# Kernel tuning notes

Hardware: AMD Instinct MI355X
Metric: run time of the kernel (lower is better)

Reference implementation:

```python
import jax, jax.numpy as jnp
import numpy as np

B, N, IN_DIM, HID, K = 32, 512, 1024, 512, 3
ALPHA = 0.2  # leaky_relu negative slope
NEG = -9e15


def setup_inputs() -> dict:
    key = jax.random.key(0)
    ks = jax.random.split(key, 7)
    hidden_states = jax.random.normal(ks[0], (B, N, IN_DIM), jnp.float32)
    adj = (jax.random.uniform(ks[1], (B, 3, N, N)) < 0.05).astype(jnp.float32)
    W_all = jax.random.normal(ks[2], (3, K, IN_DIM, HID), jnp.float32) * 0.02
    a_all = jax.random.normal(ks[3], (3, K, 2 * HID, 1), jnp.float32) * 0.02
    wawa_w = jax.random.normal(ks[4], (HID, 100), jnp.float32) * 0.05
    wawa_b = jnp.zeros((100,), jnp.float32)
    ctx_w = jax.random.normal(ks[5], (100, 1), jnp.float32) * 0.05
    return {"hidden_states": hidden_states, "adj": adj, "W_all": W_all,
            "a_all": a_all, "wawa_w": wawa_w, "wawa_b": wawa_b, "ctx_w": ctx_w}


def _gat(adj_m, x, W, a):
    # e_ij = leaky_relu(cat[h_i, h_j] @ a) == leaky_relu(h_i@a1 + h_j@a2)
    h = jnp.einsum('bnf,fh->bnh', x, W)           # [B,N,HID]
    f1 = jnp.einsum('bnh,ho->bno', h, a[:HID])    # [B,N,1]
    f2 = jnp.einsum('bnh,ho->bno', h, a[HID:])    # [B,N,1]
    e = jax.nn.leaky_relu(f1 + jnp.swapaxes(f2, 1, 2), negative_slope=ALPHA)  # [B,N,N]
    att = jnp.where(adj_m > 0, e, NEG)
    att = jax.nn.softmax(att, axis=2)
    return jnp.einsum('bnm,bmh->bnh', att, h)


def reference(hidden_states, adj, W_all, a_all, wawa_w, wawa_b, ctx_w):
    adj_a, adj_b, adj_c = adj[:, 0], adj[:, 1], adj[:, 2]
    pa, pb, pc = adj_a, adj_b, adj_c  # matmuls(A, k) = A^(k+1)
    hs = []
    for layer in range(K):
        if layer > 0:
            pa = jnp.matmul(pa, adj_a)
            pb = jnp.matmul(pb, adj_b)
            pc = jnp.matmul(pc, adj_c)
        h_layer = (_gat(pa, hidden_states, W_all[0, layer], a_all[0, layer])
                   + _gat(pb, hidden_states, W_all[1, layer], a_all[1, layer])
                   + _gat(pc, hidden_states, W_all[2, layer], a_all[2, layer]))
        hs.append(h_layer)
    # attention-based combination over the K orders
    s = [jnp.einsum('bnc,co->bno', jnp.tanh(jnp.einsum('bnh,hc->bnc', h, wawa_w) + wawa_b), ctx_w)
         for h in hs]                              # each [B,N,1]
    vs = jax.nn.softmax(jnp.concatenate(s, axis=2), axis=2)  # [B,N,K]
    h_stack = jnp.stack(hs, axis=2)                # [B,N,K,HID]
    return jnp.sum(vs[..., None] * h_stack, axis=2)  # [B,N,HID]
```

## Files before the change

kernel.cpp:

```cpp
#include <hip/hip_runtime.h>
#include <hip/hip_bf16.h>

typedef short v8s __attribute__((ext_vector_type(8)));
typedef float v4f __attribute__((ext_vector_type(4)));
typedef unsigned long long u64;

#define ALPHA 0.2f

__device__ inline unsigned short f32_bf16(float x){
    unsigned int u = __float_as_uint(x);
    unsigned int r = (u + 0x7fffu + ((u >> 16) & 1u)) >> 16;
    return (unsigned short)r;
}
__device__ inline float bf16_f32(unsigned short s){
    return __uint_as_float(((unsigned int)s) << 16);
}
__device__ inline v4f mfma16(v8s a, v8s b, v4f c){
    return __builtin_amdgcn_mfma_f32_16x16x32_bf16(a, b, c, 0, 0, 0);
}
__device__ inline void gload16(const unsigned short* g, short* l){
    __builtin_amdgcn_global_load_lds((const __attribute__((address_space(1))) unsigned int*)g,
                                     (__attribute__((address_space(3))) unsigned int*)l,
                                     16, 0, 0);
}


__global__ void k_convert_x(const float* __restrict__ x, v8s* __restrict__ out, int n8){
    int i = blockIdx.x * 256 + threadIdx.x;
    if (i >= n8) return;
    const float4* p = (const float4*)x + (size_t)i * 2;
    float4 a = p[0], b = p[1];
    v8s r;
    r[0] = (short)f32_bf16(a.x); r[1] = (short)f32_bf16(a.y);
    r[2] = (short)f32_bf16(a.z); r[3] = (short)f32_bf16(a.w);
    r[4] = (short)f32_bf16(b.x); r[5] = (short)f32_bf16(b.y);
    r[6] = (short)f32_bf16(b.z); r[7] = (short)f32_bf16(b.w);
    out[i] = r;
}

__global__ void k_transpose_w(const float* __restrict__ W, unsigned short* __restrict__ Wt){
    __shared__ float tile[32][33];
    int g = blockIdx.z, k0 = blockIdx.x * 32, h0 = blockIdx.y * 32;
    int tx = threadIdx.x, ty = threadIdx.y;
    #pragma unroll
    for (int i = 0; i < 4; ++i)
        tile[ty + i*8][tx] = W[((size_t)g*1024 + k0 + ty + i*8)*512 + h0 + tx];
    __syncthreads();
    #pragma unroll
    for (int i = 0; i < 4; ++i){
        int h = ty + i*8;
        Wt[((size_t)g*512 + h0 + h)*1024 + k0 + tx] = f32_bf16(tile[tx][h]);
    }
}

__global__ void k_wawat(const float* __restrict__ w, unsigned short* __restrict__ wt){
    int i = blockIdx.x * 256 + threadIdx.x;
    if (i >= 128 * 512) return;
    int c = i >> 9, k = i & 511;
    wt[i] = (c < 100) ? f32_bf16(w[k*100 + c]) : (unsigned short)0;
}


__global__ __launch_bounds__(256) void k_bits(const float* __restrict__ adj,
                                              u64* __restrict__ bits){
    int row = blockIdx.x * 4 + (threadIdx.x >> 6);
    int t = row >> 14, b = (row >> 9) & 31, i = row & 511;
    const float* src = adj + (((size_t)b*3 + t)*512 + i)*512;
    int lane = threadIdx.x & 63;
    #pragma unroll
    for (int w = 0; w < 8; ++w){
        u64 word = __ballot(src[w*64 + lane] > 0.5f);
        if (lane == 0) bits[(size_t)row*8 + w] = word;
    }
}

__global__ __launch_bounds__(256) void k_boolmm(const u64* __restrict__ prev,
                                                const u64* __restrict__ base,
                                                u64* __restrict__ out){
    int row = blockIdx.x * 256 + threadIdx.x;
    if (row >= 49152) return;
    int tb = row >> 9;
    const u64* pr = prev + (size_t)row * 8;
    const u64* bb = base + ((size_t)tb << 9) * 8;
    ulonglong2 a0 = {0,0}, a1 = {0,0}, a2 = {0,0}, a3 = {0,0};
    #pragma unroll
    for (int w = 0; w < 8; ++w){
        u64 m = pr[w];
        const u64* bw = bb + (size_t)(w << 6) * 8;
        while (m){
            int k = __builtin_ctzll(m);
            m &= m - 1;
            const ulonglong2* br = (const ulonglong2*)(bw + (size_t)k * 8);
            ulonglong2 b0 = br[0], b1 = br[1], b2 = br[2], b3 = br[3];
            a0.x |= b0.x; a0.y |= b0.y;
            a1.x |= b1.x; a1.y |= b1.y;
            a2.x |= b2.x; a2.y |= b2.y;
            a3.x |= b3.x; a3.y |= b3.y;
        }
    }
    ulonglong2* op = (ulonglong2*)(out + (size_t)row * 8);
    op[0] = a0; op[1] = a1; op[2] = a2; op[3] = a3;
}

__global__ __launch_bounds__(256, 4) void k_gemm_h(
    const unsigned short* __restrict__ Wt, const unsigned short* __restrict__ Xb,
    unsigned short* __restrict__ Ht, const float* __restrict__ aall,
    float* __restrict__ f1p, float* __restrict__ f2p, int l)
{
    __shared__ __align__(16) short As[128*32];
    __shared__ __align__(16) short As2[128*32];
    __shared__ __align__(16) short Bs[128*32];
    __shared__ __align__(16) short Bs2[128*32];
    const int bn = blockIdx.x, bm = blockIdx.y, t = blockIdx.z;
    const int g = t*3 + l;
    const int tid = threadIdx.x;
    const int lane = tid & 63, wave = tid >> 6;
    const int wr = wave >> 1, wc = wave & 1;
    const int fr = lane & 15, fq = lane >> 4;
    const int slot = fq ^ (fr & 3) ^ ((fr >> 2) & 3);

    const int srow = tid >> 2, sw = tid & 3;
    const int gw = sw ^ (srow & 3) ^ ((srow >> 2) & 3);
    const unsigned short* Ap = Wt + ((size_t)g*512 + (size_t)bm*128 + srow)*1024 + gw*8;
    const unsigned short* Bp = Xb + ((size_t)bn*128 + srow)*1024 + gw*8;
    short* AsW  = As  + wave*512;
    short* As2W = As2 + wave*512;
    short* BsW  = Bs  + wave*512;
    short* Bs2W = Bs2 + wave*512;

    v4f acc[4][4] = {};

    for (int kt = 0; kt < 16; ++kt){
        const unsigned short* a0 = Ap + kt*64;
        const unsigned short* b0 = Bp + kt*64;
        gload16(a0,                AsW);
        gload16(a0 + 64*1024,      AsW  + 2048);
        gload16(b0,                BsW);
        gload16(b0 + 64*1024,      BsW  + 2048);
        gload16(a0 + 32,           As2W);
        gload16(a0 + 32 + 64*1024, As2W + 2048);
        gload16(b0 + 32,           Bs2W);
        gload16(b0 + 32 + 64*1024, Bs2W + 2048);
        __syncthreads();
        {
            v8s af[4], bf[4];
            #pragma unroll
            for (int i = 0; i < 4; ++i) af[i] = *(const v8s*)&As[(wr*64 + i*16 + fr)*32 + slot*8];
            #pragma unroll
            for (int i = 0; i < 4; ++i) bf[i] = *(const v8s*)&Bs[(wc*64 + i*16 + fr)*32 + slot*8];
            #pragma unroll
            for (int i = 0; i < 4; ++i)
                #pragma unroll
                for (int j = 0; j < 4; ++j)
                    acc[i][j] = mfma16(af[i], bf[j], acc[i][j]);
        }
        {
            v8s af[4], bf[4];
            #pragma unroll
            for (int i = 0; i < 4; ++i) af[i] = *(const v8s*)&As2[(wr*64 + i*16 + fr)*32 + slot*8];
            #pragma unroll
            for (int i = 0; i < 4; ++i) bf[i] = *(const v8s*)&Bs2[(wc*64 + i*16 + fr)*32 + slot*8];
            #pragma unroll
            for (int i = 0; i < 4; ++i)
                #pragma unroll
                for (int j = 0; j < 4; ++j)
                    acc[i][j] = mfma16(af[i], bf[j], acc[i][j]);
        }
        __syncthreads();
    }
    #pragma unroll
    for (int i = 0; i < 4; ++i){
        const int h = bm*128 + wr*64 + i*16 + fq*4;
        #pragma unroll
        for (int j = 0; j < 4; ++j){
            const int mc = bn*128 + wc*64 + j*16 + fr;
            unsigned short* dst = Ht + ((size_t)t*512 + h)*16384 + mc;
            #pragma unroll
            for (int rg = 0; rg < 4; ++rg)
                dst[(size_t)rg*16384] = f32_bf16(acc[i][j][rg]);
        }
    }
    const float* a1 = aall + ((size_t)t*3 + l)*1024;
    const float* a2 = a1 + 512;
    float s1[4] = {0.f,0.f,0.f,0.f}, s2[4] = {0.f,0.f,0.f,0.f};
    #pragma unroll
    for (int i = 0; i < 4; ++i){
        #pragma unroll
        for (int rg = 0; rg < 4; ++rg){
            const int h = bm*128 + wr*64 + i*16 + fq*4 + rg;
            const float c1 = a1[h], c2 = a2[h];
            #pragma unroll
            for (int j = 0; j < 4; ++j){
                s1[j] += acc[i][j][rg]*c1;
                s2[j] += acc[i][j][rg]*c2;
            }
        }
    }
    #pragma unroll
    for (int j = 0; j < 4; ++j){
        s1[j] += __shfl_xor(s1[j], 16); s1[j] += __shfl_xor(s1[j], 32);
        s2[j] += __shfl_xor(s2[j], 16); s2[j] += __shfl_xor(s2[j], 32);
    }
    float* scr = (float*)As;
    __syncthreads();
    if (fq == 0){
        #pragma unroll
        for (int j = 0; j < 4; ++j){
            scr[(((wr*2 + wc)*4 + j)*16 + fr)*2 + 0] = s1[j];
            scr[(((wr*2 + wc)*4 + j)*16 + fr)*2 + 1] = s2[j];
        }
    }
    __syncthreads();
    if (tid < 256){
        const int which = tid & 1, fr2 = (tid >> 1) & 15, j2 = (tid >> 5) & 3,
                  wc2 = (tid >> 7) & 1;
        const float v = scr[(((0*2 + wc2)*4 + j2)*16 + fr2)*2 + which]
                      + scr[(((1*2 + wc2)*4 + j2)*16 + fr2)*2 + which];
        const int m = bn*128 + wc2*64 + j2*16 + fr2;
        float* dst = which ? f2p : f1p;
        dst[((size_t)bm*3 + t)*16384 + m] = v;
    }
}

__global__ __launch_bounds__(256) void k_soft(
    const float* __restrict__ f1p, const float* __restrict__ f2p,
    const u64* __restrict__ maskP, unsigned short* __restrict__ att)
{
    const int row = blockIdx.x * 4 + (threadIdx.x >> 6);
    const int lane = threadIdx.x & 63;
    const int tb = row >> 9;
    const int t = tb >> 5, b = tb & 31;
    const int m1 = b*512 + (row & 511);
    float f1v = 0.f;
    #pragma unroll
    for (int bm = 0; bm < 4; ++bm)
        f1v += f1p[((size_t)bm*3 + t)*16384 + m1];
    const u64 mword = maskP[(size_t)row*8 + (lane >> 3)];
    const unsigned int mbits = (unsigned int)((mword >> ((lane & 7)*8)) & 0xffu);
    const int m2 = b*512 + lane*8;
    float f2v[8] = {0.f,0.f,0.f,0.f,0.f,0.f,0.f,0.f};
    #pragma unroll
    for (int bm = 0; bm < 4; ++bm){
        const float4* fp = (const float4*)(f2p + ((size_t)bm*3 + t)*16384 + m2);
        float4 fa = fp[0], fb = fp[1];
        f2v[0] += fa.x; f2v[1] += fa.y; f2v[2] += fa.z; f2v[3] += fa.w;
        f2v[4] += fb.x; f2v[5] += fb.y; f2v[6] += fb.z; f2v[7] += fb.w;
    }
    float p[8];
    float sm = 0.f;
    #pragma unroll
    for (int u = 0; u < 8; ++u){
        float e = f1v + f2v[u];
        e = (e >= 0.f) ? e : ALPHA*e;
        float pe = (mbits & (1u << u)) ? __expf(e) : 0.f;
        p[u] = pe; sm += pe;
    }
    sm += __shfl_xor(sm, 1);  sm += __shfl_xor(sm, 2);  sm += __shfl_xor(sm, 4);
    sm += __shfl_xor(sm, 8);  sm += __shfl_xor(sm, 16); sm += __shfl_xor(sm, 32);
    const float rinv = 1.f / (sm + 1e-30f);
    v8s pk;
    #pragma unroll
    for (int u = 0; u < 8; ++u) pk[u] = (short)f32_bf16(p[u] * rinv);
    *(v8s*)&att[(size_t)row*512 + lane*8] = pk;
}

__global__ __launch_bounds__(256, 4) void k_pv(
    const unsigned short* __restrict__ att, const unsigned short* __restrict__ Ht,
    unsigned short* __restrict__ hlb)
{
    __shared__ __align__(16) short As[128*32];
    __shared__ __align__(16) short As2[128*32];
    __shared__ __align__(16) short Bs[128*32];
    __shared__ __align__(16) short Bs2[128*32];
    const int b = blockIdx.x, hc = blockIdx.y, rt = blockIdx.z;
    const int tid = threadIdx.x;
    const int lane = tid & 63, wave = tid >> 6;
    const int wr = wave >> 1, wc = wave & 1;
    const int fr = lane & 15, fq = lane >> 4;
    const int slot = fq ^ (fr & 3) ^ ((fr >> 2) & 3);
    const int srow = tid >> 2, sw = tid & 3;
    const int gw = sw ^ (srow & 3) ^ ((srow >> 2) & 3);
    short* AsW  = As  + wave*512;
    short* As2W = As2 + wave*512;
    short* BsW  = Bs  + wave*512;
    short* Bs2W = Bs2 + wave*512;

    v4f acc[4][4] = {};

    for (int t = 0; t < 3; ++t){
        const unsigned short* Ap = att + ((size_t)((t*32 + b)*512 + rt*128 + srow))*512 + gw*8;
        const unsigned short* Bp = Ht + ((size_t)t*512 + hc*128 + srow)*16384 + (size_t)b*512 + gw*8;
        for (int kk = 0; kk < 8; ++kk){
            const unsigned short* a0 = Ap + kk*64;
            const unsigned short* b0 = Bp + kk*64;
            gload16(a0,                         AsW);
            gload16(a0 + 64*512,                AsW  + 2048);
            gload16(b0,                         BsW);
            gload16(b0 + (size_t)64*16384,      BsW  + 2048);
            gload16(a0 + 32,                    As2W);
            gload16(a0 + 32 + 64*512,           As2W + 2048);
            gload16(b0 + 32,                    Bs2W);
            gload16(b0 + 32 + (size_t)64*16384, Bs2W + 2048);
            __syncthreads();
            {
                v8s af[4], bf[4];
                #pragma unroll
                for (int i = 0; i < 4; ++i) af[i] = *(const v8s*)&As[(wr*64 + i*16 + fr)*32 + slot*8];
                #pragma unroll
                for (int j = 0; j < 4; ++j) bf[j] = *(const v8s*)&Bs[(wc*64 + j*16 + fr)*32 + slot*8];
                #pragma unroll
                for (int i = 0; i < 4; ++i)
                    #pragma unroll
                    for (int j = 0; j < 4; ++j)
                        acc[i][j] = mfma16(af[i], bf[j], acc[i][j]);
            }
            {
                v8s af[4], bf[4];
                #pragma unroll
                for (int i = 0; i < 4; ++i) af[i] = *(const v8s*)&As2[(wr*64 + i*16 + fr)*32 + slot*8];
                #pragma unroll
                for (int j = 0; j < 4; ++j) bf[j] = *(const v8s*)&Bs2[(wc*64 + j*16 + fr)*32 + slot*8];
                #pragma unroll
                for (int i = 0; i < 4; ++i)
                    #pragma unroll
                    for (int j = 0; j < 4; ++j)
                        acc[i][j] = mfma16(af[i], bf[j], acc[i][j]);
            }
            __syncthreads();
        }
    }
    #pragma unroll
    for (int i = 0; i < 4; ++i){
        const int r = rt*128 + wr*64 + i*16 + fq*4;
        #pragma unroll
        for (int j = 0; j < 4; ++j){
            const int h = hc*128 + wc*64 + j*16 + fr;
            unsigned short* d1 = hlb + ((size_t)b*512 + r)*512 + h;
            #pragma unroll
            for (int rg = 0; rg < 4; ++rg)
                d1[(size_t)rg*512] = f32_bf16(acc[i][j][rg]);
        }
    }
}

__global__ __launch_bounds__(256) void k_gemm_s(
    const unsigned short* __restrict__ Hb, const unsigned short* __restrict__ Wwt,
    const float* __restrict__ wb, const float* __restrict__ cw,
    float* __restrict__ s)
{
    __shared__ __align__(16) short As[128*32];
    __shared__ __align__(16) short Bs[128*32];
    const int bm = blockIdx.x;
    const int tid = threadIdx.x;
    const int lane = tid & 63, wave = tid >> 6;
    const int wr = wave >> 1, wc = wave & 1;
    const int fr = lane & 15, fq = lane >> 4;
    const int slot = fq ^ (fr & 3) ^ ((fr >> 2) & 3);
    const int srow = tid >> 2, sw = tid & 3;
    const int gw = sw ^ (srow & 3) ^ ((srow >> 2) & 3);
    const unsigned short* Ap = Hb + ((size_t)bm*128 + srow)*512 + gw*8;
    const unsigned short* Bp = Wwt + (size_t)srow*512 + gw*8;

    v4f acc[4][4] = {};
    v8s ra0 = *(const v8s*)(Ap);
    v8s ra1 = *(const v8s*)(Ap + 64*512);
    v8s rb0 = *(const v8s*)(Bp);
    v8s rb1 = *(const v8s*)(Bp + 64*512);

    for (int kt = 0; kt < 16; ++kt){
        __syncthreads();
        *(v8s*)&As[tid*8]        = ra0;
        *(v8s*)&As[tid*8 + 2048] = ra1;
        *(v8s*)&Bs[tid*8]        = rb0;
        *(v8s*)&Bs[tid*8 + 2048] = rb1;
        __syncthreads();
        if (kt + 1 < 16){
            const unsigned short* An = Ap + (kt+1)*32;
            const unsigned short* Bn = Bp + (kt+1)*32;
            ra0 = *(const v8s*)(An); ra1 = *(const v8s*)(An + 64*512);
            rb0 = *(const v8s*)(Bn); rb1 = *(const v8s*)(Bn + 64*512);
        }
        v8s af[4], bf[4];
        #pragma unroll
        for (int i = 0; i < 4; ++i) af[i] = *(const v8s*)&As[(wr*64 + i*16 + fr)*32 + slot*8];
        #pragma unroll
        for (int i = 0; i < 4; ++i) bf[i] = *(const v8s*)&Bs[(wc*64 + i*16 + fr)*32 + slot*8];
        #pragma unroll
        for (int i = 0; i < 4; ++i)
            #pragma unroll
            for (int j = 0; j < 4; ++j)
                acc[i][j] = mfma16(af[i], bf[j], acc[i][j]);
    }
    float part[4][4];
    #pragma unroll
    for (int i = 0; i < 4; ++i)
        #pragma unroll
        for (int rg = 0; rg < 4; ++rg) part[i][rg] = 0.f;
    #pragma unroll
    for (int j = 0; j < 4; ++j){
        const int c = wc*64 + j*16 + fr;
        const bool valid = (c < 100);
        const float wbc = valid ? wb[c] : 0.f;
        const float cwc = valid ? cw[c] : 0.f;
        #pragma unroll
        for (int i = 0; i < 4; ++i)
            #pragma unroll
            for (int rg = 0; rg < 4; ++rg){
                float x = acc[i][j][rg] + wbc;
                float th;
                if (x > 15.f) th = 1.f;
                else if (x < -15.f) th = -1.f;
                else { float ex = __expf(2.f*x); th = (ex - 1.f) / (ex + 1.f); }
                part[i][rg] += th * cwc;
            }
    }
    #pragma unroll
    for (int i = 0; i < 4; ++i)
        #pragma unroll
        for (int rg = 0; rg < 4; ++rg){
            float v = part[i][rg];
            v += __shfl_xor(v, 1);
            v += __shfl_xor(v, 2);
            v += __shfl_xor(v, 4);
            v += __shfl_xor(v, 8);
            part[i][rg] = v;
        }
    float* scr = (float*)As;
    __syncthreads();
    if (fr == 0){
        #pragma unroll
        for (int i = 0; i < 4; ++i)
            #pragma unroll
            for (int rg = 0; rg < 4; ++rg)
                scr[(wr*64 + i*16 + fq*4 + rg)*2 + wc] = part[i][rg];
    }
    __syncthreads();
    if (tid < 128){
        const float v = scr[tid*2] + scr[tid*2 + 1];
        const int grow = bm*128 + tid;
        s[grow] = v;
    }
}

__global__ void k_comb(const unsigned short* __restrict__ hlb, const float* __restrict__ s,
                       float* __restrict__ out)
{
    int idx = blockIdx.x * 256 + threadIdx.x;
    if (idx >= 16384*64) return;
    int m = idx >> 6, c8 = (idx & 63) << 3;
    float s0 = s[m], s1 = s[16384 + m], s2 = s[32768 + m];
    float m0 = fmaxf(s0, fmaxf(s1, s2));
    float e0 = __expf(s0-m0), e1 = __expf(s1-m0), e2 = __expf(s2-m0);
    float inv = 1.f / (e0 + e1 + e2);
    float v0 = e0*inv, v1 = e1*inv, v2 = e2*inv;
    const unsigned short* hp = hlb + (size_t)m*512 + c8;
    v8s a = *(const v8s*)hp;
    v8s bb = *(const v8s*)(hp + (size_t)16384*512);
    v8s cc = *(const v8s*)(hp + (size_t)2*16384*512);
    float o[8];
    #pragma unroll
    for (int u = 0; u < 8; ++u)
        o[u] = v0*bf16_f32((unsigned short)a[u])
             + v1*bf16_f32((unsigned short)bb[u])
             + v2*bf16_f32((unsigned short)cc[u]);
    float4* dst = (float4*)(out + (size_t)m*512 + c8);
    dst[0] = make_float4(o[0], o[1], o[2], o[3]);
    dst[1] = make_float4(o[4], o[5], o[6], o[7]);
}

extern "C" void kernel_launch(void* const* d_in, const int* in_sizes, int n_in,
                              void* d_out, int out_size, void* d_ws, size_t ws_size,
                              hipStream_t stream)
{
    (void)in_sizes; (void)n_in; (void)out_size; (void)ws_size;
    const float* hs   = (const float*)d_in[0];
    const float* adj  = (const float*)d_in[1];
    const float* W    = (const float*)d_in[2];
    const float* aall = (const float*)d_in[3];
    const float* ww   = (const float*)d_in[4];
    const float* wb   = (const float*)d_in[5];
    const float* cw   = (const float*)d_in[6];
    float* out = (float*)d_out;
    char* ws = (char*)d_ws;

    unsigned short* Xb  = (unsigned short*)(ws);
    unsigned short* Wt  = (unsigned short*)(ws + 33554432);
    unsigned short* Wwt = (unsigned short*)(ws + 42991616);
    u64* bits           = (u64*)(ws + 43122688);
    u64* P2             = (u64*)(ws + 46268416);
    u64* P3             = (u64*)(ws + 49414144);
    unsigned short* Ht  = (unsigned short*)(ws + 52559872);
    float* f1p          = (float*)(ws + 103284736);
    float* f2p          = (float*)(ws + 104071168);
    unsigned short* att = (unsigned short*)(ws + 104857600);
    unsigned short* hlb = (unsigned short*)(ws + 203948032);
    float* sbuf         = (float*)(ws + 52559872);

    k_convert_x<<<8192, 256, 0, stream>>>(hs, (v8s*)Xb, 2097152);
    k_transpose_w<<<dim3(32,16,9), dim3(32,8), 0, stream>>>(W, Wt);
    k_wawat<<<256, 256, 0, stream>>>(ww, Wwt);
    k_bits<<<12288, 256, 0, stream>>>(adj, bits);
    k_boolmm<<<192, 256, 0, stream>>>(bits, bits, P2);
    k_boolmm<<<192, 256, 0, stream>>>(bits, P2, P3);

    const u64* masks[3] = {bits, P2, P3};
    for (int l = 0; l < 3; ++l){
        k_gemm_h<<<dim3(128,4,3), 256, 0, stream>>>(Wt, Xb, Ht, aall, f1p, f2p, l);
        k_soft<<<12288, 256, 0, stream>>>(f1p, f2p, masks[l], att);
        k_pv<<<dim3(32,4,4), 256, 0, stream>>>(att, Ht,
            hlb + (size_t)l*16384*512);
    }
    k_gemm_s<<<384, 256, 0, stream>>>(hlb, Wwt, wb, cw, sbuf);
    k_comb<<<4096, 256, 0, stream>>>(hlb, sbuf, out);
}
```

Baseline: 514.6 us.

## Double-buffer LDS tiles in GEMM and PV kernels to overlap loads with MFMA

Replaces the load-all-then-compute k-loop in k_gemm_h and k_pv with a two-stage ping-pong LDS pipeline. The next 32-wide k-slice is prefetched via global_load_lds while MFMAs run on the current slice, with one vmcnt wait and barrier per step. The t/kk loops in k_pv are flattened into a single 48-step pipeline, and s_setprio raises wave priority around the MFMA block. This hides global-load latency, at the cost of twice as many barriers with half the compute between each, plus hand-placed waitcnt and fences that must keep LDS hazards correct.

```diff
diff --git a/kernel.cpp b/kernel.cpp
--- a/kernel.cpp
+++ b/kernel.cpp
@@ -23,6 +23,8 @@
                                      (__attribute__((address_space(3))) unsigned int*)l,
                                      16, 0, 0);
 }
+#define VMCNT0   asm volatile("s_waitcnt vmcnt(0)" ::: "memory")
+#define CFENCE   asm volatile("" ::: "memory")
 
 
 __global__ void k_convert_x(const float* __restrict__ x, v8s* __restrict__ out, int n8){
@@ -107,10 +109,10 @@
     unsigned short* __restrict__ Ht, const float* __restrict__ aall,
     float* __restrict__ f1p, float* __restrict__ f2p, int l)
 {
-    __shared__ __align__(16) short As[128*32];
-    __shared__ __align__(16) short As2[128*32];
-    __shared__ __align__(16) short Bs[128*32];
-    __shared__ __align__(16) short Bs2[128*32];
+    __shared__ __align__(16) short As0[128*32];
+    __shared__ __align__(16) short Bs0[128*32];
+    __shared__ __align__(16) short As1[128*32];
+    __shared__ __align__(16) short Bs1[128*32];
     const int bn = blockIdx.x, bm = blockIdx.y, t = blockIdx.z;
     const int g = t*3 + l;
     const int tid = threadIdx.x;
@@ -123,50 +125,47 @@
     const int gw = sw ^ (srow & 3) ^ ((srow >> 2) & 3);
     const unsigned short* Ap = Wt + ((size_t)g*512 + (size_t)bm*128 + srow)*1024 + gw*8;
     const unsigned short* Bp = Xb + ((size_t)bn*128 + srow)*1024 + gw*8;
-    short* AsW  = As  + wave*512;
-    short* As2W = As2 + wave*512;
-    short* BsW  = Bs  + wave*512;
-    short* Bs2W = Bs2 + wave*512;
+    const int wo = wave*512;
 
     v4f acc[4][4] = {};
 
-    for (int kt = 0; kt < 16; ++kt){
-        const unsigned short* a0 = Ap + kt*64;
-        const unsigned short* b0 = Bp + kt*64;
-        gload16(a0,                AsW);
-        gload16(a0 + 64*1024,      AsW  + 2048);
-        gload16(b0,                BsW);
-        gload16(b0 + 64*1024,      BsW  + 2048);
-        gload16(a0 + 32,           As2W);
-        gload16(a0 + 32 + 64*1024, As2W + 2048);
-        gload16(b0 + 32,           Bs2W);
-        gload16(b0 + 32 + 64*1024, Bs2W + 2048);
-        __syncthreads();
-        {
-            v8s af[4], bf[4];
-            #pragma unroll
-            for (int i = 0; i < 4; ++i) af[i] = *(const v8s*)&As[(wr*64 + i*16 + fr)*32 + slot*8];
-            #pragma unroll
-            for (int i = 0; i < 4; ++i) bf[i] = *(const v8s*)&Bs[(wc*64 + i*16 + fr)*32 + slot*8];
-            #pragma unroll
-            for (int i = 0; i < 4; ++i)
-                #pragma unroll
-                for (int j = 0; j < 4; ++j)
-                    acc[i][j] = mfma16(af[i], bf[j], acc[i][j]);
-        }
-        {
-            v8s af[4], bf[4];
-            #pragma unroll
-            for (int i = 0; i < 4; ++i) af[i] = *(const v8s*)&As2[(wr*64 + i*16 + fr)*32 + slot*8];
-            #pragma unroll
-            for (int i = 0; i < 4; ++i) bf[i] = *(const v8s*)&Bs2[(wc*64 + i*16 + fr)*32 + slot*8];
-            #pragma unroll
-            for (int i = 0; i < 4; ++i)
-                #pragma unroll
-                for (int j = 0; j < 4; ++j)
-                    acc[i][j] = mfma16(af[i], bf[j], acc[i][j]);
-        }
-        __syncthreads();
+    gload16(Ap,           As0 + wo);
+    gload16(Ap + 64*1024, As0 + wo + 2048);
+    gload16(Bp,           Bs0 + wo);
+    gload16(Bp + 64*1024, Bs0 + wo + 2048);
+    VMCNT0;
+    __builtin_amdgcn_s_barrier();
+    CFENCE;
+
+    #pragma unroll 2
+    for (int kt = 0; kt < 32; ++kt){
+        short* cA = (kt & 1) ? As1 : As0;
+        short* cB = (kt & 1) ? Bs1 : Bs0;
+        if (kt + 1 < 32){
+            short* nA = (kt & 1) ? As0 : As1;
+            short* nB = (kt & 1) ? Bs0 : Bs1;
+            const unsigned short* a1 = Ap + (kt+1)*32;
+            const unsigned short* b1 = Bp + (kt+1)*32;
+            gload16(a1,           nA + wo);
+            gload16(a1 + 64*1024, nA + wo + 2048);
+            gload16(b1,           nB + wo);
+            gload16(b1 + 64*1024, nB + wo + 2048);
+        }
+        v8s af[4], bf[4];
+        #pragma unroll
+        for (int i = 0; i < 4; ++i) af[i] = *(const v8s*)&cA[(wr*64 + i*16 + fr)*32 + slot*8];
+        #pragma unroll
+        for (int i = 0; i < 4; ++i) bf[i] = *(const v8s*)&cB[(wc*64 + i*16 + fr)*32 + slot*8];
+        __builtin_amdgcn_s_setprio(1);
+        #pragma unroll
+        for (int i = 0; i < 4; ++i)
+            #pragma unroll
+            for (int j = 0; j < 4; ++j)
+                acc[i][j] = mfma16(af[i], bf[j], acc[i][j]);
+        __builtin_amdgcn_s_setprio(0);
+        VMCNT0;
+        __builtin_amdgcn_s_barrier();
+        CFENCE;
     }
     #pragma unroll
     for (int i = 0; i < 4; ++i){
@@ -180,15 +179,15 @@
                 dst[(size_t)rg*16384] = f32_bf16(acc[i][j][rg]);
         }
     }
-    const float* a1 = aall + ((size_t)t*3 + l)*1024;
-    const float* a2 = a1 + 512;
+    const float* a1v = aall + ((size_t)t*3 + l)*1024;
+    const float* a2v = a1v + 512;
     float s1[4] = {0.f,0.f,0.f,0.f}, s2[4] = {0.f,0.f,0.f,0.f};
     #pragma unroll
     for (int i = 0; i < 4; ++i){
         #pragma unroll
         for (int rg = 0; rg < 4; ++rg){
             const int h = bm*128 + wr*64 + i*16 + fq*4 + rg;
-            const float c1 = a1[h], c2 = a2[h];
+            const float c1 = a1v[h], c2 = a2v[h];
             #pragma unroll
             for (int j = 0; j < 4; ++j){
                 s1[j] += acc[i][j][rg]*c1;
@@ -201,7 +200,7 @@
         s1[j] += __shfl_xor(s1[j], 16); s1[j] += __shfl_xor(s1[j], 32);
         s2[j] += __shfl_xor(s2[j], 16); s2[j] += __shfl_xor(s2[j], 32);
     }
-    float* scr = (float*)As;
+    float* scr = (float*)As0;
     __syncthreads();
     if (fq == 0){
         #pragma unroll
@@ -268,10 +267,10 @@
     const unsigned short* __restrict__ att, const unsigned short* __restrict__ Ht,
     unsigned short* __restrict__ hlb)
 {
-    __shared__ __align__(16) short As[128*32];
-    __shared__ __align__(16) short As2[128*32];
-    __shared__ __align__(16) short Bs[128*32];
-    __shared__ __align__(16) short Bs2[128*32];
+    __shared__ __align__(16) short As0[128*32];
+    __shared__ __align__(16) short Bs0[128*32];
+    __shared__ __align__(16) short As1[128*32];
+    __shared__ __align__(16) short Bs1[128*32];
     const int b = blockIdx.x, hc = blockIdx.y, rt = blockIdx.z;
     const int tid = threadIdx.x;
     const int lane = tid & 63, wave = tid >> 6;
@@ -280,54 +279,58 @@
     const int slot = fq ^ (fr & 3) ^ ((fr >> 2) & 3);
     const int srow = tid >> 2, sw = tid & 3;
     const int gw = sw ^ (srow & 3) ^ ((srow >> 2) & 3);
-    short* AsW  = As  + wave*512;
-    short* As2W = As2 + wave*512;
-    short* BsW  = Bs  + wave*512;
-    short* Bs2W = Bs2 + wave*512;
+    const int wo = wave*512;
+
+    auto aSrc = [&](int s){
+        return att + ((size_t)(((s >> 4)*32 + b)*512 + rt*128 + srow))*512
+                   + (s & 15)*32 + gw*8;
+    };
+    auto bSrc = [&](int s){
+        return Ht + ((size_t)((s >> 4)*512 + hc*128 + srow))*16384
+                  + (size_t)b*512 + (s & 15)*32 + gw*8;
+    };
 
     v4f acc[4][4] = {};
 
-    for (int t = 0; t < 3; ++t){
-        const unsigned short* Ap = att + ((size_t)((t*32 + b)*512 + rt*128 + srow))*512 + gw*8;
-        const unsigned short* Bp = Ht + ((size_t)t*512 + hc*128 + srow)*16384 + (size_t)b*512 + gw*8;
-        for (int kk = 0; kk < 8; ++kk){
-            const unsigned short* a0 = Ap + kk*64;
-            const unsigned short* b0 = Bp + kk*64;
-            gload16(a0,                         AsW);
-            gload16(a0 + 64*512,                AsW  + 2048);
-            gload16(b0,                         BsW);
-            gload16(b0 + (size_t)64*16384,      BsW  + 2048);
-            gload16(a0 + 32,                    As2W);
-            gload16(a0 + 32 + 64*512,           As2W + 2048);
-            gload16(b0 + 32,                    Bs2W);
-            gload16(b0 + 32 + (size_t)64*16384, Bs2W + 2048);
-            __syncthreads();
-            {
-                v8s af[4], bf[4];
-                #pragma unroll
-                for (int i = 0; i < 4; ++i) af[i] = *(const v8s*)&As[(wr*64 + i*16 + fr)*32 + slot*8];
-                #pragma unroll
-                for (int j = 0; j < 4; ++j) bf[j] = *(const v8s*)&Bs[(wc*64 + j*16 + fr)*32 + slot*8];
-                #pragma unroll
-                for (int i = 0; i < 4; ++i)
-                    #pragma unroll
-                    for (int j = 0; j < 4; ++j)
-                        acc[i][j] = mfma16(af[i], bf[j], acc[i][j]);
-            }
-            {
-                v8s af[4], bf[4];
-                #pragma unroll
-                for (int i = 0; i < 4; ++i) af[i] = *(const v8s*)&As2[(wr*64 + i*16 + fr)*32 + slot*8];
-                #pragma unroll
-                for (int j = 0; j < 4; ++j) bf[j] = *(const v8s*)&Bs2[(wc*64 + j*16 + fr)*32 + slot*8];
-                #pragma unroll
-                for (int i = 0; i < 4; ++i)
-                    #pragma unroll
-                    for (int j = 0; j < 4; ++j)
-                        acc[i][j] = mfma16(af[i], bf[j], acc[i][j]);
-            }
-            __syncthreads();
-        }
+    const unsigned short* a0 = aSrc(0);
+    const unsigned short* b0 = bSrc(0);
+    gload16(a0,                    As0 + wo);
+    gload16(a0 + 64*512,           As0 + wo + 2048);
+    gload16(b0,                    Bs0 + wo);
+    gload16(b0 + (size_t)64*16384, Bs0 + wo + 2048);
+    VMCNT0;
+    __builtin_amdgcn_s_barrier();
+    CFENCE;
+
+    #pragma unroll 2
+    for (int s = 0; s < 48; ++s){
+        short* cA = (s & 1) ? As1 : As0;
+        short* cB = (s & 1) ? Bs1 : Bs0;
+        if (s + 1 < 48){
+            short* nA = (s & 1) ? As0 : As1;
+            short* nB = (s & 1) ? Bs0 : Bs1;
+            const unsigned short* a1 = aSrc(s + 1);
+            const unsigned short* b1 = bSrc(s + 1);
+            gload16(a1,                    nA + wo);
+            gload16(a1 + 64*512,           nA + wo + 2048);
+            gload16(b1,                    nB + wo);
+            gload16(b1 + (size_t)64*16384, nB + wo + 2048);
+        }
+        v8s af[4], bf[4];
+        #pragma unroll
+        for (int i = 0; i < 4; ++i) af[i] = *(const v8s*)&cA[(wr*64 + i*16 + fr)*32 + slot*8];
+        #pragma unroll
+        for (int j = 0; j < 4; ++j) bf[j] = *(const v8s*)&cB[(wc*64 + j*16 + fr)*32 + slot*8];
+        __builtin_amdgcn_s_setprio(1);
+        #pragma unroll
+        for (int i = 0; i < 4; ++i)
+            #pragma unroll
+            for (int j = 0; j < 4; ++j)
+                acc[i][j] = mfma16(af[i], bf[j], acc[i][j]);
+        __builtin_amdgcn_s_setprio(0);
+        VMCNT0;
+        __builtin_amdgcn_s_barrier();
+        CFENCE;
     }
     #pragma unroll
     for (int i = 0; i < 4; ++i){
```

Result: slower. 538.3 us (+4.6%).
